# Optimization experiments

Measured on AMD Instinct MI355X. Metric: run time of the kernel, lower is better.

Reference implementation:

```python
import jax, jax.numpy as jnp
import numpy as np
from jax import lax

HIDDEN = 51
INPUT_SIZE = 1


def setup_inputs() -> dict:
    key = jax.random.key(0)
    ks = jax.random.split(key, 7)
    B, T = 1024, 1024
    H, I = HIDDEN, INPUT_SIZE
    s_ih = 1.0 / np.sqrt(H)
    x = jax.random.normal(ks[0], (B, T), dtype=jnp.float32)
    # nn.LSTMCell params: weight_ih [4H, I], weight_hh [4H, H], biases [4H]
    W_ih = jax.random.uniform(ks[1], (4 * H, I), jnp.float32, -s_ih, s_ih)
    W_hh = jax.random.uniform(ks[2], (4 * H, H), jnp.float32, -s_ih, s_ih)
    b_ih = jax.random.uniform(ks[3], (4 * H,), jnp.float32, -s_ih, s_ih)
    b_hh = jax.random.uniform(ks[4], (4 * H,), jnp.float32, -s_ih, s_ih)
    # nn.Linear(H, 1)
    fc_w = jax.random.uniform(ks[5], (1, H), jnp.float32, -s_ih, s_ih)
    fc_b = jax.random.uniform(ks[6], (1,), jnp.float32, -s_ih, s_ih)
    return {"x": x, "W_ih": W_ih, "W_hh": W_hh, "b_ih": b_ih,
            "b_hh": b_hh, "fc_w": fc_w, "fc_b": fc_b, "future": 0}


def reference(x, W_ih, W_hh, b_ih, b_hh, fc_w, fc_b, future):
    # x: [B, T]; sequential LSTMCell over time + per-step Linear(H -> 1).
    B, T = x.shape
    H = W_hh.shape[1]

    def step(carry, x_t):
        h, c = carry  # [B, H]
        gates = x_t @ W_ih.T + b_ih + h @ W_hh.T + b_hh  # [B, 4H]
        i, f, g, o = jnp.split(gates, 4, axis=-1)  # PyTorch gate order i,f,g,o
        i = jax.nn.sigmoid(i)
        f = jax.nn.sigmoid(f)
        g = jnp.tanh(g)
        o = jax.nn.sigmoid(o)
        c = f * c + i * g
        h = o * jnp.tanh(c)
        out = h @ fc_w.T + fc_b  # [B, 1]
        return (h, c), out

    h0 = jnp.zeros((B, H), x.dtype)
    c0 = jnp.zeros((B, H), x.dtype)
    xs = x.T[:, :, None]  # [T, B, 1]
    (_, _), outs = lax.scan(step, (h0, c0), xs)  # outs: [T, B, 1]
    return outs[:, :, 0].T  # [B, T], matches torch.cat(outputs, dim=1)
```

## Files before the change

### kernel.cpp

```cpp
#include <hip/hip_runtime.h>


#define HID 51
#define SEQ_T 1024
#define NKW 52

static __device__ __forceinline__ float lane_bcast(float v, int lane) {
    return __int_as_float(__builtin_amdgcn_readlane(__float_as_int(v), lane));
}
static __device__ __forceinline__ float fast_sigmoid(float x) {
    float e = __builtin_amdgcn_exp2f(x * -1.44269504088896340736f);
    return __builtin_amdgcn_rcpf(1.0f + e);
}
static __device__ __forceinline__ float fast_tanh(float x) {
    float e = __builtin_amdgcn_exp2f(x * 2.88539008177792681472f);
    return 1.0f - 2.0f * __builtin_amdgcn_rcpf(e + 1.0f);
}

#define FMAC(acc, h, w) \
    asm("v_fmac_f32 %0, %1, %2" : "+v"(acc) : "v"(h), "v"(w))

__global__ __launch_bounds__(128)
__attribute__((amdgpu_waves_per_eu(2, 2)))
void lstm_duo32_kernel(
    const float* __restrict__ x,
    const float* __restrict__ W_ih,
    const float* __restrict__ W_hh,
    const float* __restrict__ b_ih,
    const float* __restrict__ b_hh,
    const float* __restrict__ fc_w,
    const float* __restrict__ fc_b,
    float* __restrict__ out)
{
    const int b = blockIdx.x;
    const int tid = threadIdx.x;
    const int w = tid >> 6;
    const int l = tid & 63;
    const bool act = (l < HID);

    __shared__ __align__(16) float hrep[2][64];
    __shared__ float2 axch[2][2][64];
    __shared__ float pbuf[64][65];

    const int gA = 2 * w;
    const int gB = 2 * w + 1;

    float wA[NKW], wB[NKW];
#pragma unroll
    for (int k = 0; k < NKW; ++k) {
        const bool v = act && (k < HID);
        wA[k] = v ? W_hh[(gA * HID + l) * HID + k] : 0.f;
        wB[k] = v ? W_hh[(gB * HID + l) * HID + k] : 0.f;
        asm volatile("" : "+v"(wA[k]), "+v"(wB[k]));
    }
    float bA = 0.f, bB = 0.f, wxA = 0.f, wxB = 0.f, fcw = 0.f;
    if (act) {
        bA = b_ih[gA * HID + l] + b_hh[gA * HID + l];
        bB = b_ih[gB * HID + l] + b_hh[gB * HID + l];
        wxA = W_ih[gA * HID + l];
        wxB = W_ih[gB * HID + l];
        fcw = fc_w[l];
    }
    const float fcb = fc_b[0];
    float c = 0.f;

    hrep[w][l] = 0.f;
    __syncthreads();

    const float4* __restrict__ hq4 = (const float4*)(&hrep[w][0]);

#pragma unroll 1
    for (int t0 = 0; t0 < SEQ_T; t0 += 64) {
        const float xv = x[b * SEQ_T + t0 + l];

#pragma unroll 1
        for (int i = 0; i < 64; ++i) {
            const float xt = lane_bcast(xv, i);
            float sA0 = fmaf(xt, wxA, bA), sA1 = 0.f;
            float sB0 = fmaf(xt, wxB, bB), sB1 = 0.f;
#pragma unroll
            for (int q = 0; q < 13; ++q) {
                const float4 h4 = hq4[q];
                FMAC(sA0, h4.x, wA[4 * q + 0]);
                FMAC(sB0, h4.x, wB[4 * q + 0]);
                FMAC(sA1, h4.y, wA[4 * q + 1]);
                FMAC(sB1, h4.y, wB[4 * q + 1]);
                FMAC(sA0, h4.z, wA[4 * q + 2]);
                FMAC(sB0, h4.z, wB[4 * q + 2]);
                FMAC(sA1, h4.w, wA[4 * q + 3]);
                FMAC(sB1, h4.w, wB[4 * q + 3]);
            }
            const float sA = sA0 + sA1;
            const float sB = sB0 + sB1;

            float aA, aB;
            if (w == 0) { aA = fast_sigmoid(sA); aB = fast_sigmoid(sB); }
            else        { aA = fast_tanh(sA);    aB = fast_sigmoid(sB); }
            const int par = i & 1;
            axch[par][w][l] = make_float2(aA, aB);
            __syncthreads();
            const float2 oth = axch[par][1 - w][l];

            float ig, fg, gg, og;
            if (w == 0) { ig = aA;    fg = aB;    gg = oth.x; og = oth.y; }
            else        { ig = oth.x; fg = oth.y; gg = aA;    og = aB; }

            c = fmaf(fg, c, ig * gg);
            const float hn = og * fast_tanh(c);
            hrep[w][l] = hn;

            if (w == 0) pbuf[l][i] = hn * fcw;
        }

        if (w == 0) {
            float s2r = 0.f;
#pragma unroll
            for (int k = 0; k < HID; ++k) s2r += pbuf[k][l];
            out[b * SEQ_T + t0 + l] = s2r + fcb;
        }
    }
}

extern "C" void kernel_launch(void* const* d_in, const int* in_sizes, int n_in,
                              void* d_out, int out_size, void* d_ws, size_t ws_size,
                              hipStream_t stream) {
    (void)in_sizes; (void)n_in; (void)d_ws; (void)ws_size; (void)out_size;
    const float* x    = (const float*)d_in[0];
    const float* W_ih = (const float*)d_in[1];
    const float* W_hh = (const float*)d_in[2];
    const float* b_ih = (const float*)d_in[3];
    const float* b_hh = (const float*)d_in[4];
    const float* fc_w = (const float*)d_in[5];
    const float* fc_b = (const float*)d_in[6];
    float* out = (float*)d_out;

    lstm_duo32_kernel<<<dim3(1024), dim3(128), 0, stream>>>(
        x, W_ih, W_hh, b_ih, b_hh, fc_w, fc_b, out);
}
```

Baseline: 568.3 us.

## Split LSTM gates across four waves, one gate row per lane

Each block now runs four waves instead of two, and each wave owns one gate (i, f, g or o), so every lane holds 51 weights instead of 102. This halves the FMA chain per step and the register pressure, and allows four waves per EU. The cost is that each step's barrier now synchronises four waves, and each lane reads all four activations from shared memory instead of exchanging with one partner. The removed __syncthreads after hrep initialisation may also introduce a race on the first step.

```diff
diff --git a/kernel.cpp b/kernel.cpp
--- a/kernel.cpp
+++ b/kernel.cpp
@@ -3,7 +3,6 @@
 
 #define HID 51
 #define SEQ_T 1024
-#define NKW 52
 
 static __device__ __forceinline__ float lane_bcast(float v, int lane) {
     return __int_as_float(__builtin_amdgcn_readlane(__float_as_int(v), lane));
@@ -17,12 +16,9 @@
     return 1.0f - 2.0f * __builtin_amdgcn_rcpf(e + 1.0f);
 }
 
-#define FMAC(acc, h, w) \
-    asm("v_fmac_f32 %0, %1, %2" : "+v"(acc) : "v"(h), "v"(w))
-
-__global__ __launch_bounds__(128)
-__attribute__((amdgpu_waves_per_eu(2, 2)))
-void lstm_duo32_kernel(
+__global__ __launch_bounds__(256)
+__attribute__((amdgpu_waves_per_eu(4, 4)))
+void lstm_gate4_kernel(
     const float* __restrict__ x,
     const float* __restrict__ W_ih,
     const float* __restrict__ W_hh,
@@ -34,40 +30,30 @@
 {
     const int b = blockIdx.x;
     const int tid = threadIdx.x;
-    const int w = tid >> 6;
+    const int g = tid >> 6;
     const int l = tid & 63;
-    const bool act = (l < HID);
+    const bool on = (l < HID);
 
-    __shared__ __align__(16) float hrep[2][64];
-    __shared__ float2 axch[2][2][64];
+    __shared__ __align__(16) float hrep[4][64];
+    __shared__ float actb[2][4][64];
     __shared__ float pbuf[64][65];
 
-    const int gA = 2 * w;
-    const int gB = 2 * w + 1;
+    float wq[HID + 1];
+#pragma unroll
+    for (int k = 0; k < HID; ++k) {
+        wq[k] = on ? W_hh[(g * HID + l) * HID + k] : 0.f;
+        asm volatile("" : "+v"(wq[k]));
+    }
+    wq[HID] = 0.f;
 
-    float wA[NKW], wB[NKW];
-#pragma unroll
-    for (int k = 0; k < NKW; ++k) {
-        const bool v = act && (k < HID);
-        wA[k] = v ? W_hh[(gA * HID + l) * HID + k] : 0.f;
-        wB[k] = v ? W_hh[(gB * HID + l) * HID + k] : 0.f;
-        asm volatile("" : "+v"(wA[k]), "+v"(wB[k]));
-    }
-    float bA = 0.f, bB = 0.f, wxA = 0.f, wxB = 0.f, fcw = 0.f;
-    if (act) {
-        bA = b_ih[gA * HID + l] + b_hh[gA * HID + l];
-        bB = b_ih[gB * HID + l] + b_hh[gB * HID + l];
-        wxA = W_ih[gA * HID + l];
-        wxB = W_ih[gB * HID + l];
-        fcw = fc_w[l];
-    }
-    const float fcb = fc_b[0];
+    const float bias = on ? b_ih[g * HID + l] + b_hh[g * HID + l] : 0.f;
+    const float wx   = on ? W_ih[g * HID + l] : 0.f;
+    const float fcw  = on ? fc_w[l] : 0.f;
+    const float fcb  = fc_b[0];
     float c = 0.f;
 
-    hrep[w][l] = 0.f;
-    __syncthreads();
-
-    const float4* __restrict__ hq4 = (const float4*)(&hrep[w][0]);
+    hrep[g][l] = 0.f;
+    const float4* __restrict__ hq4 = (const float4*)(&hrep[g][0]);
 
 #pragma unroll 1
     for (int t0 = 0; t0 < SEQ_T; t0 += 64) {
@@ -76,43 +62,34 @@
 #pragma unroll 1
         for (int i = 0; i < 64; ++i) {
             const float xt = lane_bcast(xv, i);
-            float sA0 = fmaf(xt, wxA, bA), sA1 = 0.f;
-            float sB0 = fmaf(xt, wxB, bB), sB1 = 0.f;
+            float s0 = fmaf(xt, wx, bias), s1 = 0.f;
 #pragma unroll
             for (int q = 0; q < 13; ++q) {
                 const float4 h4 = hq4[q];
-                FMAC(sA0, h4.x, wA[4 * q + 0]);
-                FMAC(sB0, h4.x, wB[4 * q + 0]);
-                FMAC(sA1, h4.y, wA[4 * q + 1]);
-                FMAC(sB1, h4.y, wB[4 * q + 1]);
-                FMAC(sA0, h4.z, wA[4 * q + 2]);
-                FMAC(sB0, h4.z, wB[4 * q + 2]);
-                FMAC(sA1, h4.w, wA[4 * q + 3]);
-                FMAC(sB1, h4.w, wB[4 * q + 3]);
+                s0 = fmaf(h4.x, wq[4 * q + 0], s0);
+                s1 = fmaf(h4.y, wq[4 * q + 1], s1);
+                s0 = fmaf(h4.z, wq[4 * q + 2], s0);
+                s1 = fmaf(h4.w, wq[4 * q + 3], s1);
             }
-            const float sA = sA0 + sA1;
-            const float sB = sB0 + sB1;
+            const float s = s0 + s1;
 
-            float aA, aB;
-            if (w == 0) { aA = fast_sigmoid(sA); aB = fast_sigmoid(sB); }
-            else        { aA = fast_tanh(sA);    aB = fast_sigmoid(sB); }
+            const float a = (g == 2) ? fast_tanh(s) : fast_sigmoid(s);
             const int par = i & 1;
-            axch[par][w][l] = make_float2(aA, aB);
+            actb[par][g][l] = a;
             __syncthreads();
-            const float2 oth = axch[par][1 - w][l];
 
-            float ig, fg, gg, og;
-            if (w == 0) { ig = aA;    fg = aB;    gg = oth.x; og = oth.y; }
-            else        { ig = oth.x; fg = oth.y; gg = aA;    og = aB; }
-
+            const float ig = actb[par][0][l];
+            const float fg = actb[par][1][l];
+            const float gg = actb[par][2][l];
+            const float og = actb[par][3][l];
             c = fmaf(fg, c, ig * gg);
             const float hn = og * fast_tanh(c);
-            hrep[w][l] = hn;
+            hrep[g][l] = hn;
 
-            if (w == 0) pbuf[l][i] = hn * fcw;
+            if (g == 0) pbuf[l][i] = hn * fcw;
         }
 
-        if (w == 0) {
+        if (g == 0) {
             float s2r = 0.f;
 #pragma unroll
             for (int k = 0; k < HID; ++k) s2r += pbuf[k][l];
@@ -134,6 +111,6 @@
     const float* fc_b = (const float*)d_in[6];
     float* out = (float*)d_out;
 
-    lstm_duo32_kernel<<<dim3(1024), dim3(128), 0, stream>>>(
+    lstm_gate4_kernel<<<dim3(1024), dim3(256), 0, stream>>>(
         x, W_ih, W_hh, b_ih, b_hh, fc_w, fc_b, out);
 }
```

Result: slower. 652.2 us (+14.8%).
